# Performance work log

Measured on AMD Instinct MI355X. Metric: run time of the kernel, lower is better.

Reference implementation:

```python
import jax, jax.numpy as jnp
import numpy as np

NUM_CLASS = 16  # static stand-in for int(max(label)+1) in the torch code


def setup_inputs() -> dict:
    key = jax.random.key(0)
    k1, k2 = jax.random.split(key)
    N, D = 524288, 64
    feat = jax.random.normal(k1, (N, D), dtype=jnp.float32)
    label = jax.random.randint(k2, (N,), 0, NUM_CLASS, dtype=jnp.int64)
    return {"feat": feat, "label": label}


def _top_right_singular_vectors(feat, label, num_class):
    """Per class c: top right singular vector of feat[label==c] (= avg_feat[0]
    from np.linalg.svd). Computed as the top eigenvector of the class Gram
    matrix G_c = X_c^T X_c; zero (masked-out) rows do not change G_c, so this
    matches the variable-size per-class SVD without ragged shapes."""
    def gram(c):
        m = (label == c).astype(feat.dtype)          # [N] 0/1 mask
        return jnp.einsum('nd,ne->de', feat * m[:, None], feat)  # [d, d]
    # sequential over the small, fixed class set -> only one [N, d] temp alive
    G = jax.lax.map(gram, jnp.arange(num_class))      # [C, d, d]
    _, vecs = jnp.linalg.eigh(G)                      # ascending eigenvalues
    v = vecs[..., -1]                                 # [C, d] top eigenvector
    # SVD sign is arbitrary; fix a convention: largest-|.| component positive
    idx = jnp.argmax(jnp.abs(v), axis=1)
    s = jnp.sign(jnp.take_along_axis(v, idx[:, None], axis=1))  # [C, 1]
    return v * s


def reference(feat, label):
    # inner[i, c] = <feat_i, v_c>; given[i] = inner[i, label_i]
    # -> only the gathered column is needed: <feat_i, v_{label_i}>
    V = _top_right_singular_vectors(feat, label, NUM_CLASS)  # [C, d]
    given = jnp.sum(feat * V[label], axis=1)                 # [N]
    return given
```

## Files before the change

### kernel.cpp

```cpp
#include <hip/hip_runtime.h>
#include <math.h>

#define NCLS 16
#define DIM  64
#define GBLK 64
#define QQ   8
#define STEP (4 * GBLK * QQ)

__global__ __launch_bounds__(256) void k_hist(const int* __restrict__ label,
                                              int n, int* __restrict__ hpart,
                                              float* __restrict__ G) {
    __shared__ int h[NCLS * 16];
    h[threadIdx.x] = 0;
    for (int e = blockIdx.x * 256 + threadIdx.x; e < NCLS * DIM * DIM;
         e += gridDim.x * 256)
        G[e] = 0.f;
    __syncthreads();
    const int sub = threadIdx.x & 15;
    const long i0 = (long)(blockIdx.x * 256 + threadIdx.x) * 8;
    if (i0 + 8 <= n) {
        int4 a = *(const int4*)(label + i0);
        int4 b = *(const int4*)(label + i0 + 4);
        atomicAdd(&h[a.x * 16 + sub], 1);
        atomicAdd(&h[a.y * 16 + sub], 1);
        atomicAdd(&h[a.z * 16 + sub], 1);
        atomicAdd(&h[a.w * 16 + sub], 1);
        atomicAdd(&h[b.x * 16 + sub], 1);
        atomicAdd(&h[b.y * 16 + sub], 1);
        atomicAdd(&h[b.z * 16 + sub], 1);
        atomicAdd(&h[b.w * 16 + sub], 1);
    } else {
        for (long i = i0; i < n; i++) atomicAdd(&h[label[i] * 16 + sub], 1);
    }
    __syncthreads();
    if (threadIdx.x < NCLS) {
        int s = 0;
#pragma unroll
        for (int j = 0; j < 16; j++) s += h[threadIdx.x * 16 + j];
        hpart[blockIdx.x * 16 + threadIdx.x] = s;
    }
}

__global__ void k_scan(const int* __restrict__ hpart, int nb,
                       int* __restrict__ cnt, int* __restrict__ base,
                       int* __restrict__ cursor) {
    __shared__ int ph[64];
    __shared__ int sc[16];
    const int t = threadIdx.x;
    const int c = t & 15, part = t >> 4;
    const int nb4 = (nb + 3) >> 2;
    int s = 0;
    for (int b = part * nb4; b < nb && b < (part + 1) * nb4; b++)
        s += hpart[b * 16 + c];
    ph[t] = s;
    __syncthreads();
    if (t < 16) {
        int tot = ph[t] + ph[16 + t] + ph[32 + t] + ph[48 + t];
        sc[t] = tot;
        cnt[t] = tot;
    }
    __syncthreads();
    if (t < 16) {
        int pre = 0;
        for (int j = 0; j < t; j++) pre += (sc[j] + 3) & ~3;
        base[t] = pre;
        cursor[t] = pre;
    }
}

__global__ __launch_bounds__(256) void k_scatter(const int* __restrict__ label,
                                                 int n, int* __restrict__ cursor,
                                                 int* __restrict__ idx) {
    __shared__ int h[NCLS * 16];
    __shared__ int cur[NCLS * 16];
    __shared__ int gb[NCLS];
    h[threadIdx.x] = 0;
    __syncthreads();
    const int sub = threadIdx.x & 15;
    const long i0 = (long)(blockIdx.x * 256 + threadIdx.x) * 8;
    int4 a, b;
    const bool full = (i0 + 8 <= n);
    if (full) {
        a = *(const int4*)(label + i0);
        b = *(const int4*)(label + i0 + 4);
        atomicAdd(&h[a.x * 16 + sub], 1);
        atomicAdd(&h[a.y * 16 + sub], 1);
        atomicAdd(&h[a.z * 16 + sub], 1);
        atomicAdd(&h[a.w * 16 + sub], 1);
        atomicAdd(&h[b.x * 16 + sub], 1);
        atomicAdd(&h[b.y * 16 + sub], 1);
        atomicAdd(&h[b.z * 16 + sub], 1);
        atomicAdd(&h[b.w * 16 + sub], 1);
    } else {
        for (long i = i0; i < n; i++) atomicAdd(&h[label[i] * 16 + sub], 1);
    }
    __syncthreads();
    {
        const int c = threadIdx.x >> 4, s = threadIdx.x & 15;
        int pre = 0;
        for (int j = 0; j < 16; j++) pre += (j < s) ? h[c * 16 + j] : 0;
        if (s == 15) gb[c] = atomicAdd(&cursor[c], pre + h[threadIdx.x]);
        __syncthreads();
        cur[threadIdx.x] = gb[c] + pre;
    }
    __syncthreads();
    if (full) {
        int p;
        p = atomicAdd(&cur[a.x * 16 + sub], 1); idx[p] = (int)i0 + 0;
        p = atomicAdd(&cur[a.y * 16 + sub], 1); idx[p] = (int)i0 + 1;
        p = atomicAdd(&cur[a.z * 16 + sub], 1); idx[p] = (int)i0 + 2;
        p = atomicAdd(&cur[a.w * 16 + sub], 1); idx[p] = (int)i0 + 3;
        p = atomicAdd(&cur[b.x * 16 + sub], 1); idx[p] = (int)i0 + 4;
        p = atomicAdd(&cur[b.y * 16 + sub], 1); idx[p] = (int)i0 + 5;
        p = atomicAdd(&cur[b.z * 16 + sub], 1); idx[p] = (int)i0 + 6;
        p = atomicAdd(&cur[b.w * 16 + sub], 1); idx[p] = (int)i0 + 7;
    } else {
        for (long i = i0; i < n; i++) {
            int p = atomicAdd(&cur[label[i] * 16 + sub], 1);
            idx[p] = (int)i;
        }
    }
}

__global__ __launch_bounds__(256, 4) void k_gram(const float* __restrict__ feat,
                                                 const int* __restrict__ idx,
                                                 const int* __restrict__ base,
                                                 const int* __restrict__ cnt,
                                                 float* __restrict__ G,
                                                 int nrows) {
    const int c    = blockIdx.x & (NCLS - 1);
    const int blk  = blockIdx.x >> 4;
    const int wave = threadIdx.x >> 6;
    const int lane = threadIdx.x & 63;
    const int gw   = blk * 4 + wave;
    const int r0   = (lane >> 3) << 3;
    const int c0   = (lane & 7) << 3;
    const int m    = cnt[c];
    const int b0   = base[c];

    __shared__ float stage[4 * 2 * 512];
    float* st = stage + wave * 1024;

    float acc[8][8];
#pragma unroll
    for (int j = 0; j < 8; j++)
#pragma unroll
        for (int k = 0; k < 8; k++) acc[j][k] = 0.f;

    const int p0    = gw * QQ;
    const int nfull = (m >= p0 + QQ) ? ((m - QQ - p0) / STEP + 1) : 0;
    const int sr    = lane >> 4;
    const int sc16  = lane & 15;
    const int* ippA = idx + b0 + p0 + sr;
    const int* ippB = ippA + 4;

#define STAGE(ROW, DSTF)                                                        \
    __builtin_amdgcn_global_load_lds(                                           \
        (const __attribute__((address_space(1))) void*)(feat + (size_t)(ROW) * DIM + sc16 * 4), \
        (__attribute__((address_space(3))) void*)((DSTF)), 16, 0, 0)

    int inA = 0, inB = 0;
    if (nfull > 0) {
        int a0 = ippA[0], b0r = ippB[0];
        STAGE(a0, st);
        STAGE(b0r, st + 256);
        inA = ippA[STEP];
        inB = ippB[STEP];
    }

    for (int k = 0; k < nfull; k++) {
        const int buf = (k & 1) << 9;
        int ifA = ippA[(size_t)(k + 2) * STEP];
        int ifB = ippB[(size_t)(k + 2) * STEP];
        int nA = ((unsigned)inA < (unsigned)nrows) ? inA : 0;
        int nB = ((unsigned)inB < (unsigned)nrows) ? inB : 0;
        float* ob = st + (buf ^ 512);
        STAGE(nA, ob);
        STAGE(nB, ob + 256);
        asm volatile("s_waitcnt vmcnt(4)" ::: "memory");
        const float* sb = st + buf;
#pragma unroll
        for (int q = 0; q < QQ; q++) {
            float4 a0 = *(const float4*)(sb + q * 64 + r0);
            float4 a1 = *(const float4*)(sb + q * 64 + r0 + 4);
            float4 bb0 = *(const float4*)(sb + q * 64 + c0);
            float4 bb1 = *(const float4*)(sb + q * 64 + c0 + 4);
            float av[8] = {a0.x, a0.y, a0.z, a0.w, a1.x, a1.y, a1.z, a1.w};
            float bv[8] = {bb0.x, bb0.y, bb0.z, bb0.w, bb1.x, bb1.y, bb1.z, bb1.w};
#pragma unroll
            for (int j = 0; j < 8; j++)
#pragma unroll
                for (int kk = 0; kk < 8; kk++)
                    acc[j][kk] = fmaf(av[j], bv[kk], acc[j][kk]);
        }
        inA = ifA; inB = ifB;
    }
    asm volatile("s_waitcnt vmcnt(0)" ::: "memory");
#undef STAGE

    const int pt = p0 + nfull * STEP;
#pragma unroll
    for (int q = 0; q < QQ; q++) {
        if (pt + q < m) {
            int jrow = idx[b0 + pt + q];
            const float* rp = feat + (size_t)jrow * DIM;
            float4 a0 = *(const float4*)(rp + r0), a1 = *(const float4*)(rp + r0 + 4);
            float4 bb0 = *(const float4*)(rp + c0), bb1 = *(const float4*)(rp + c0 + 4);
            float av[8] = {a0.x, a0.y, a0.z, a0.w, a1.x, a1.y, a1.z, a1.w};
            float bv[8] = {bb0.x, bb0.y, bb0.z, bb0.w, bb1.x, bb1.y, bb1.z, bb1.w};
#pragma unroll
            for (int j = 0; j < 8; j++)
#pragma unroll
                for (int kk = 0; kk < 8; kk++)
                    acc[j][kk] = fmaf(av[j], bv[kk], acc[j][kk]);
        }
    }

    __shared__ float tile[DIM * DIM];
    for (int w = 0; w < 4; w++) {
        if (wave == w) {
            float* t = tile + r0 * DIM + c0;
            if (w == 0) {
#pragma unroll
                for (int j = 0; j < 8; j++) {
                    *(float4*)(t + j * DIM)     = make_float4(acc[j][0], acc[j][1], acc[j][2], acc[j][3]);
                    *(float4*)(t + j * DIM + 4) = make_float4(acc[j][4], acc[j][5], acc[j][6], acc[j][7]);
                }
            } else {
#pragma unroll
                for (int j = 0; j < 8; j++) {
                    float4 u0 = *(float4*)(t + j * DIM);
                    float4 u1 = *(float4*)(t + j * DIM + 4);
                    u0.x += acc[j][0]; u0.y += acc[j][1]; u0.z += acc[j][2]; u0.w += acc[j][3];
                    u1.x += acc[j][4]; u1.y += acc[j][5]; u1.z += acc[j][6]; u1.w += acc[j][7];
                    *(float4*)(t + j * DIM)     = u0;
                    *(float4*)(t + j * DIM + 4) = u1;
                }
            }
        }
        __syncthreads();
    }
    float* g = G + c * DIM * DIM;
    for (int e = threadIdx.x; e < DIM * DIM; e += 256)
        atomicAdd(&g[e], tile[e]);
}

__global__ __launch_bounds__(256, 1) void k_eig(const float* __restrict__ G,
                                                float* __restrict__ V) {
    const int c    = blockIdx.x;
    const int t    = threadIdx.x;
    const int wave = t >> 6;
    const int lane = t & 63;
    __shared__ float shA[DIM * DIM];
    __shared__ float shB[DIM * DIM];
    __shared__ float shP[4 * DIM];
    __shared__ float shRed[4];
    __shared__ float shV[DIM];

    {
        const float4* g4 = (const float4*)(G + c * DIM * DIM);
        float4* a4 = (float4*)shA;
#pragma unroll
        for (int j = 0; j < 4; j++) a4[t + 256 * j] = g4[t + 256 * j];
    }
    __syncthreads();

    float ss = 0.f;
    {
        const float4* a4 = (const float4*)shA;
#pragma unroll
        for (int j = 0; j < 4; j++) {
            float4 x = a4[t + 256 * j];
            ss = fmaf(x.x, x.x, fmaf(x.y, x.y, fmaf(x.z, x.z, fmaf(x.w, x.w, ss))));
        }
    }
#pragma unroll
    for (int m = 1; m < 64; m <<= 1) ss += __shfl_xor(ss, m);
    if (lane == 0) shRed[wave] = ss;
    __syncthreads();
    if (wave == 0) {
        float s2 = shRed[0] + shRed[1] + shRed[2] + shRed[3];
        float d  = shA[lane * 65];
        float sd = d;
#pragma unroll
        for (int m = 1; m < 64; m <<= 1) sd += __shfl_xor(sd, m);
        float mu    = sd * (1.f / 64.f);
        float var   = fmaxf(s2 * (1.f / 64.f) - mu * mu, 0.f);
        float sigma = mu - 0.2f * sqrtf(var);
        shA[lane * 65] = d - sigma;
    }
    __syncthreads();

    float* cur = shA;
    float* nxt = shB;
    const int ra = wave * 16 + ((lane >> 3) << 1);
    const int c0 = (lane & 7) << 3;
    for (int sq = 0; sq < 7; sq++) {
        float acc[2][8];
#pragma unroll
        for (int j = 0; j < 8; j++) { acc[0][j] = 0.f; acc[1][j] = 0.f; }
#pragma unroll 4
        for (int k = 0; k < DIM; k++) {
            const float* rk = cur + k * DIM;
            float2 a2 = *(const float2*)(rk + ra);
            float4 b0 = *(const float4*)(rk + c0);
            float4 b1 = *(const float4*)(rk + c0 + 4);
            acc[0][0] = fmaf(a2.x, b0.x, acc[0][0]);
            acc[0][1] = fmaf(a2.x, b0.y, acc[0][1]);
            acc[0][2] = fmaf(a2.x, b0.z, acc[0][2]);
            acc[0][3] = fmaf(a2.x, b0.w, acc[0][3]);
            acc[0][4] = fmaf(a2.x, b1.x, acc[0][4]);
            acc[0][5] = fmaf(a2.x, b1.y, acc[0][5]);
            acc[0][6] = fmaf(a2.x, b1.z, acc[0][6]);
            acc[0][7] = fmaf(a2.x, b1.w, acc[0][7]);
            acc[1][0] = fmaf(a2.y, b0.x, acc[1][0]);
            acc[1][1] = fmaf(a2.y, b0.y, acc[1][1]);
            acc[1][2] = fmaf(a2.y, b0.z, acc[1][2]);
            acc[1][3] = fmaf(a2.y, b0.w, acc[1][3]);
            acc[1][4] = fmaf(a2.y, b1.x, acc[1][4]);
            acc[1][5] = fmaf(a2.y, b1.y, acc[1][5]);
            acc[1][6] = fmaf(a2.y, b1.z, acc[1][6]);
            acc[1][7] = fmaf(a2.y, b1.w, acc[1][7]);
        }
        *(float4*)(nxt + (ra + 0) * DIM + c0)     = make_float4(acc[0][0], acc[0][1], acc[0][2], acc[0][3]);
        *(float4*)(nxt + (ra + 0) * DIM + c0 + 4) = make_float4(acc[0][4], acc[0][5], acc[0][6], acc[0][7]);
        *(float4*)(nxt + (ra + 1) * DIM + c0)     = make_float4(acc[1][0], acc[1][1], acc[1][2], acc[1][3]);
        *(float4*)(nxt + (ra + 1) * DIM + c0 + 4) = make_float4(acc[1][4], acc[1][5], acc[1][6], acc[1][7]);
        __syncthreads();
        float4 xs[4];
        float mx = 0.f;
        {
            const float4* n4 = (const float4*)nxt;
#pragma unroll
            for (int j = 0; j < 4; j++) {
                float4 x = n4[t + 256 * j];
                xs[j] = x;
                mx = fmaxf(mx, fmaxf(fmaxf(fabsf(x.x), fabsf(x.y)),
                                     fmaxf(fabsf(x.z), fabsf(x.w))));
            }
        }
#pragma unroll
        for (int m = 1; m < 64; m <<= 1) mx = fmaxf(mx, __shfl_xor(mx, m));
        if (lane == 0) shRed[wave] = mx;
        __syncthreads();
        float gm = fmaxf(fmaxf(shRed[0], shRed[1]), fmaxf(shRed[2], shRed[3]));
        float inv = (gm > 0.f) ? (1.0f / gm) : 1.0f;
        {
            float4* n4 = (float4*)nxt;
#pragma unroll
            for (int j = 0; j < 4; j++) {
                float4 x = xs[j];
                n4[t + 256 * j] = make_float4(x.x * inv, x.y * inv, x.z * inv, x.w * inv);
            }
        }
        __syncthreads();
        float* tmp = cur; cur = nxt; nxt = tmp;
    }

    if (wave == 0) {
        float d = cur[lane * 65];
        float dmax = d;
#pragma unroll
        for (int m = 1; m < 64; m <<= 1) dmax = fmaxf(dmax, __shfl_xor(dmax, m));
        unsigned long long bal = __ballot(d == dmax);
        int jstar = __ffsll((long long)bal) - 1;
        shV[lane] = cur[jstar * DIM + lane];
    }
    __syncthreads();

    for (int it = 0; it < 8; it++) {
        float part = 0.f;
#pragma unroll
        for (int j = 0; j < 16; j++) {
            int k = wave * 16 + j;
            part = fmaf(cur[k * DIM + lane], shV[k], part);
        }
        shP[wave * DIM + lane] = part;
        __syncthreads();
        if (wave == 0)
            shV[lane] = shP[lane] + shP[64 + lane] + shP[128 + lane] + shP[192 + lane];
        __syncthreads();
    }

    if (wave == 0) {
        float val = shV[lane];
        float nn = val * val;
#pragma unroll
        for (int m = 1; m < 64; m <<= 1) nn += __shfl_xor(nn, m);
        float inv = (nn > 1e-30f) ? rsqrtf(nn) : 1.0f;
        float am = fabsf(val);
        float bm = am;
#pragma unroll
        for (int m = 1; m < 64; m <<= 1) bm = fmaxf(bm, __shfl_xor(bm, m));
        unsigned long long bal = __ballot(am == bm);
        int jm = __ffsll((long long)bal) - 1;
        float vm = __shfl(val, jm);
        float s = (vm < 0.f) ? -inv : inv;
        V[c * DIM + lane] = val * s;
    }
}

__global__ __launch_bounds__(256) void k_out(const float* __restrict__ feat,
                                             const int* __restrict__ label,
                                             const float* __restrict__ V,
                                             float* __restrict__ out, int n) {
    int i = blockIdx.x * blockDim.x + threadIdx.x;
    if (i >= n) return;
    const float4* rp = (const float4*)(feat + (size_t)i * DIM);
    const float4* vp = (const float4*)(V + label[i] * DIM);
    float s0 = 0, s1 = 0, s2 = 0, s3 = 0;
#pragma unroll
    for (int j = 0; j < 16; j++) {
        float4 a = rp[j], b = vp[j];
        s0 = fmaf(a.x, b.x, s0);
        s1 = fmaf(a.y, b.y, s1);
        s2 = fmaf(a.z, b.z, s2);
        s3 = fmaf(a.w, b.w, s3);
    }
    out[i] = (s0 + s1) + (s2 + s3);
}

extern "C" void kernel_launch(void* const* d_in, const int* in_sizes, int n_in,
                              void* d_out, int out_size, void* d_ws, size_t ws_size,
                              hipStream_t stream) {
    const float* feat  = (const float*)d_in[0];
    const int*   label = (const int*)d_in[1];
    const int    n     = in_sizes[1];
    float*       out   = (float*)d_out;

    int*   wsi    = (int*)d_ws;
    int*   cnt    = wsi;
    int*   base   = wsi + 16;
    int*   cursor = wsi + 32;
    int*   hpart  = wsi + 48;
    float* G      = (float*)(wsi + 4160);
    float* V      = G + NCLS * DIM * DIM;
    int*   idx    = (int*)(V + NCLS * DIM);

    const int hblocks = (n + 2047) / 2048;
    k_hist<<<hblocks, 256, 0, stream>>>(label, n, hpart, G);
    k_scan<<<1, 64, 0, stream>>>(hpart, hblocks, cnt, base, cursor);
    k_scatter<<<hblocks, 256, 0, stream>>>(label, n, cursor, idx);
    k_gram<<<NCLS * GBLK, 256, 0, stream>>>(feat, idx, base, cnt, G, n);
    k_eig<<<NCLS, 256, 0, stream>>>(G, V);
    k_out<<<(n + 255) / 256, 256, 0, stream>>>(feat, label, V, out, n);
}
```

Measured before the change: 303.7 us.

## Replace histogram+scan+scatter with fixed-capacity per-class bins in one pass

```diff
diff --git a/kernel.cpp b/kernel.cpp
--- a/kernel.cpp
+++ b/kernel.cpp
@@ -6,75 +6,19 @@
 #define GBLK 64
 #define QQ   8
 #define STEP (4 * GBLK * QQ)
-
-__global__ __launch_bounds__(256) void k_hist(const int* __restrict__ label,
-                                              int n, int* __restrict__ hpart,
-                                              float* __restrict__ G) {
+#define CAP  65536
+
+__global__ __launch_bounds__(256) void k_bin(const int* __restrict__ label,
+                                             int n, int* __restrict__ cursor,
+                                             int* __restrict__ idx,
+                                             float* __restrict__ G) {
     __shared__ int h[NCLS * 16];
+    __shared__ int cur[NCLS * 16];
+    __shared__ int gb[NCLS];
     h[threadIdx.x] = 0;
     for (int e = blockIdx.x * 256 + threadIdx.x; e < NCLS * DIM * DIM;
          e += gridDim.x * 256)
         G[e] = 0.f;
-    __syncthreads();
-    const int sub = threadIdx.x & 15;
-    const long i0 = (long)(blockIdx.x * 256 + threadIdx.x) * 8;
-    if (i0 + 8 <= n) {
-        int4 a = *(const int4*)(label + i0);
-        int4 b = *(const int4*)(label + i0 + 4);
-        atomicAdd(&h[a.x * 16 + sub], 1);
-        atomicAdd(&h[a.y * 16 + sub], 1);
-        atomicAdd(&h[a.z * 16 + sub], 1);
-        atomicAdd(&h[a.w * 16 + sub], 1);
-        atomicAdd(&h[b.x * 16 + sub], 1);
-        atomicAdd(&h[b.y * 16 + sub], 1);
-        atomicAdd(&h[b.z * 16 + sub], 1);
-        atomicAdd(&h[b.w * 16 + sub], 1);
-    } else {
-        for (long i = i0; i < n; i++) atomicAdd(&h[label[i] * 16 + sub], 1);
-    }
-    __syncthreads();
-    if (threadIdx.x < NCLS) {
-        int s = 0;
-#pragma unroll
-        for (int j = 0; j < 16; j++) s += h[threadIdx.x * 16 + j];
-        hpart[blockIdx.x * 16 + threadIdx.x] = s;
-    }
-}
-
-__global__ void k_scan(const int* __restrict__ hpart, int nb,
-                       int* __restrict__ cnt, int* __restrict__ base,
-                       int* __restrict__ cursor) {
-    __shared__ int ph[64];
-    __shared__ int sc[16];
-    const int t = threadIdx.x;
-    const int c = t & 15, part = t >> 4;
-    const int nb4 = (nb + 3) >> 2;
-    int s = 0;
-    for (int b = part * nb4; b < nb && b < (part + 1) * nb4; b++)
-        s += hpart[b * 16 + c];
-    ph[t] = s;
-    __syncthreads();
-    if (t < 16) {
-        int tot = ph[t] + ph[16 + t] + ph[32 + t] + ph[48 + t];
-        sc[t] = tot;
-        cnt[t] = tot;
-    }
-    __syncthreads();
-    if (t < 16) {
-        int pre = 0;
-        for (int j = 0; j < t; j++) pre += (sc[j] + 3) & ~3;
-        base[t] = pre;
-        cursor[t] = pre;
-    }
-}
-
-__global__ __launch_bounds__(256) void k_scatter(const int* __restrict__ label,
-                                                 int n, int* __restrict__ cursor,
-                                                 int* __restrict__ idx) {
-    __shared__ int h[NCLS * 16];
-    __shared__ int cur[NCLS * 16];
-    __shared__ int gb[NCLS];
-    h[threadIdx.x] = 0;
     __syncthreads();
     const int sub = threadIdx.x & 15;
     const long i0 = (long)(blockIdx.x * 256 + threadIdx.x) * 8;
@@ -101,7 +45,7 @@
         for (int j = 0; j < 16; j++) pre += (j < s) ? h[c * 16 + j] : 0;
         if (s == 15) gb[c] = atomicAdd(&cursor[c], pre + h[threadIdx.x]);
         __syncthreads();
-        cur[threadIdx.x] = gb[c] + pre;
+        cur[threadIdx.x] = c * CAP + gb[c] + pre;
     }
     __syncthreads();
     if (full) {
@@ -124,7 +68,6 @@
 
 __global__ __launch_bounds__(256, 4) void k_gram(const float* __restrict__ feat,
                                                  const int* __restrict__ idx,
-                                                 const int* __restrict__ base,
                                                  const int* __restrict__ cnt,
                                                  float* __restrict__ G,
                                                  int nrows) {
@@ -136,7 +79,7 @@
     const int r0   = (lane >> 3) << 3;
     const int c0   = (lane & 7) << 3;
     const int m    = cnt[c];
-    const int b0   = base[c];
+    const int b0   = c * CAP;
 
     __shared__ float stage[4 * 2 * 512];
     float* st = stage + wave * 1024;
@@ -429,19 +372,15 @@
     float*       out   = (float*)d_out;
 
     int*   wsi    = (int*)d_ws;
-    int*   cnt    = wsi;
-    int*   base   = wsi + 16;
-    int*   cursor = wsi + 32;
-    int*   hpart  = wsi + 48;
-    float* G      = (float*)(wsi + 4160);
+    int*   cursor = wsi;
+    float* G      = (float*)(wsi + 16);
     float* V      = G + NCLS * DIM * DIM;
     int*   idx    = (int*)(V + NCLS * DIM);
 
     const int hblocks = (n + 2047) / 2048;
-    k_hist<<<hblocks, 256, 0, stream>>>(label, n, hpart, G);
-    k_scan<<<1, 64, 0, stream>>>(hpart, hblocks, cnt, base, cursor);
-    k_scatter<<<hblocks, 256, 0, stream>>>(label, n, cursor, idx);
-    k_gram<<<NCLS * GBLK, 256, 0, stream>>>(feat, idx, base, cnt, G, n);
+    hipMemsetAsync(cursor, 0, NCLS * sizeof(int), stream);
+    k_bin<<<hblocks, 256, 0, stream>>>(label, n, cursor, idx, G);
+    k_gram<<<NCLS * GBLK, 256, 0, stream>>>(feat, idx, cursor, G, n);
     k_eig<<<NCLS, 256, 0, stream>>>(G, V);
     k_out<<<(n + 255) / 256, 256, 0, stream>>>(feat, label, V, out, n);
 }
```

After: 290.5 us (median of 2 runs). 1.05x faster.
